# Kernel optimization log

Hardware: AMD Instinct MI355X
Metric: run time of the kernel (lower is better)

Reference implementation:

```python
import jax, jax.numpy as jnp
import numpy as np

N = 50000        # nodes
E = 800000       # edges (before self-loops)
F_IN = 128       # num_features
HID = 32         # hidden_size per head
HEADS = 4
CLS = 40         # num_classes
NEG_SLOPE = 0.2  # PyG GATConv default leaky_relu slope


def setup_inputs() -> dict:
    key = jax.random.key(0)
    ks = jax.random.split(key, 10)
    s = lambda k, sh: (jax.random.normal(k, sh, jnp.float32) * 0.05)
    x = jax.random.normal(ks[0], (N, F_IN), jnp.float32)
    edge_index = jax.random.randint(ks[1], (2, E), 0, N, dtype=jnp.int64)
    W1 = s(ks[2], (F_IN, HEADS * HID))
    att_src1 = s(ks[3], (HEADS, HID))
    att_dst1 = s(ks[4], (HEADS, HID))
    b1 = jnp.zeros((HEADS * HID,), jnp.float32)
    W2 = s(ks[5], (HEADS * HID, CLS))
    att_src2 = s(ks[6], (1, CLS))
    att_dst2 = s(ks[7], (1, CLS))
    b2 = jnp.zeros((CLS,), jnp.float32)
    return {"x": x, "edge_index": edge_index, "W1": W1, "att_src1": att_src1,
            "att_dst1": att_dst1, "b1": b1, "W2": W2, "att_src2": att_src2,
            "att_dst2": att_dst2, "b2": b2}


def _add_self_loops(edge_index, num_nodes):
    ar = jnp.arange(num_nodes, dtype=edge_index.dtype)
    loops = jnp.stack([ar, ar])
    return jnp.concatenate([edge_index, loops], axis=1)


def _gat_conv(x, edge_index, W, a_src, a_dst, bias, heads, concat):
    """PyG GATConv (eval mode, additive attention, self-loops already added)."""
    n = x.shape[0]
    src, dst = edge_index[0], edge_index[1]
    h = (x @ W).reshape(n, heads, -1)                 # [N, H, C]
    a_s = jnp.einsum('nhc,hc->nh', h, a_src)          # [N, H]
    a_d = jnp.einsum('nhc,hc->nh', h, a_dst)          # [N, H]
    e = jax.nn.leaky_relu(a_s[src] + a_d[dst], NEG_SLOPE)   # [E', H]
    m = jax.ops.segment_max(e, dst, num_segments=n)   # segment softmax over dst
    ex = jnp.exp(e - m[dst])
    den = jax.ops.segment_sum(ex, dst, num_segments=n)
    alpha = ex / den[dst]                             # [E', H]
    out = jax.ops.segment_sum(h[src] * alpha[:, :, None], dst, num_segments=n)
    out = out.reshape(n, -1) if concat else out.mean(axis=1)
    return out + bias


def reference(x, edge_index, W1, att_src1, att_dst1, b1, W2, att_src2, att_dst2, b2):
    ei = _add_self_loops(edge_index, x.shape[0])
    # dropout p=0 in eval -> identity
    h = jax.nn.relu(_gat_conv(x, ei, W1, att_src1, att_dst1, b1, HEADS, True))
    out = _gat_conv(h, ei, W2, att_src2, att_dst2, b2, 1, True)  # heads=1
    return out
```

## Files before the change

kernel.cpp:

```cpp
#include <hip/hip_runtime.h>
#include <cstdint>

#define NODES 50000
#define FIN   128
#define C1    128
#define HEADS 4
#define HID   32
#define CLS   40
#define SLOPE 0.2f

#define NBUCK ((NODES + 255) >> 8)
#define EPB 2048
#define BCAP 8192

__device__ __forceinline__ float lrelu(float v) { return v > 0.f ? v : SLOPE * v; }

__device__ __forceinline__ unsigned short f2bf(float f) {
    union { float f; unsigned u; } v; v.f = f;
    unsigned u = v.u;
    return (unsigned short)((u + 0x7FFFu + ((u >> 16) & 1u)) >> 16);
}
__device__ __forceinline__ float bf2f(unsigned short b) {
    union { unsigned u; float f; } v; v.u = ((unsigned)b) << 16;
    return v.f;
}
__device__ __forceinline__ float bflo(unsigned u) {
    union { unsigned x; float f; } v; v.x = u << 16; return v.f;
}
__device__ __forceinline__ float bfhi(unsigned u) {
    union { unsigned x; float f; } v; v.x = u & 0xffff0000u; return v.f;
}
__device__ __forceinline__ unsigned cvtpk(float a, float b) {
    unsigned r;
    asm("v_cvt_pk_bf16_f32 %0, %1, %2" : "=v"(r) : "v"(a), "v"(b));
    return r;
}

typedef __attribute__((ext_vector_type(8))) short bf16x8;
typedef __attribute__((ext_vector_type(4))) float f32x4;
typedef __attribute__((ext_vector_type(4), aligned(4))) int int4a;
typedef __attribute__((ext_vector_type(2), aligned(4))) int int2a;

__device__ __forceinline__ void acc8(float w, uint4 p, float* ac) {
    ac[0] = fmaf(w, bflo(p.x), ac[0]); ac[1] = fmaf(w, bfhi(p.x), ac[1]);
    ac[2] = fmaf(w, bflo(p.y), ac[2]); ac[3] = fmaf(w, bfhi(p.y), ac[3]);
    ac[4] = fmaf(w, bflo(p.z), ac[4]); ac[5] = fmaf(w, bfhi(p.z), ac[5]);
    ac[6] = fmaf(w, bflo(p.w), ac[6]); ac[7] = fmaf(w, bfhi(p.w), ac[7]);
}

__global__ __launch_bounds__(256) void k_prep(const float* __restrict__ W1,
                                              const float* __restrict__ W2,
                                              unsigned short* __restrict__ w1t,
                                              unsigned short* __restrict__ w2t,
                                              int* __restrict__ bwp) {
    const int b = blockIdx.x, t = threadIdx.x;
    if (b < 8) {
        __shared__ unsigned short Tb[16][136];
        const int n0 = b * 16;
        const int k = t & 127, g = t >> 7;
#pragma unroll
        for (int i = 0; i < 8; i++)
            Tb[g * 8 + i][k] = f2bf(W1[(size_t)k * C1 + n0 + g * 8 + i]);
        __syncthreads();
        {
            int nl = t >> 4, k8 = (t & 15) * 8;
            *(uint4*)(w1t + (n0 + nl) * 128 + k8) = *(uint4*)(&Tb[nl][k8]);
        }
    } else {
        for (int p = t; p < CLS * 128; p += 256) {
            int n = p >> 7, k = p & 127;
            w2t[n * 128 + k] = f2bf(W2[(size_t)k * CLS + n]);
        }
        if (t < NBUCK) bwp[t] = t * BCAP;
    }
}

__global__ __launch_bounds__(256) void k_front(const float* __restrict__ X,
                                               const unsigned short* __restrict__ w1t,
                                               const float* __restrict__ AS,
                                               const float* __restrict__ AD,
                                               unsigned short* __restrict__ h1b,
                                               float* __restrict__ as1,
                                               float* __restrict__ ad1,
                                               const int* __restrict__ src,
                                               const int* __restrict__ dst, int E,
                                               int* __restrict__ bwp,
                                               int* __restrict__ tmp, int GB1) {
    __shared__ unsigned short Asm[64][136];
    __shared__ unsigned short Wt[128][136];
    __shared__ int cnt[NBUCK];
    __shared__ int bbs[NBUCK];
    const int t = threadIdx.x;

    if (blockIdx.x >= GB1) {
        for (int i = t; i < NBUCK; i += 256) cnt[i] = 0;
        __syncthreads();
        const int e0 = (blockIdx.x - GB1) * EPB;
        int v[8], rb[8];
#pragma unroll
        for (int k = 0; k < 8; k++) {
            int e = e0 + k * 256 + t;
            rb[k] = -1;
            if (e < E) {
                int d = dst[e], s = src[e];
                int b = d >> 8;
                int r = atomicAdd(&cnt[b], 1);
                v[k] = (s << 8) | (d & 255);
                rb[k] = (r << 8) | b;
            }
        }
        __syncthreads();
        for (int i = t; i < NBUCK; i += 256) {
            int c = cnt[i];
            bbs[i] = c ? atomicAdd(&bwp[i], c) : 0;
        }
        __syncthreads();
#pragma unroll
        for (int k = 0; k < 8; k++) {
            if (rb[k] >= 0) {
                int b = rb[k] & 255;
                int r = rb[k] >> 8;
                tmp[bbs[b] + r] = v[k];
            }
        }
        return;
    }

    const int row0 = blockIdx.x * 64;
#pragma unroll
    for (int i = 0; i < 8; i++) {
        int p = i * 256 + t;
        int n = p >> 4, k8 = (p & 15) * 8;
        *(uint4*)(&Wt[n][k8]) = *(const uint4*)(w1t + n * 128 + k8);
    }
    {
        int r = t >> 2, c0 = (t & 3) * 32;
        int gr = row0 + r;
        if (gr < NODES) {
#pragma unroll
            for (int i = 0; i < 4; i++) {
                float4 va = *(const float4*)(X + (size_t)gr * FIN + c0 + i * 8);
                float4 vb = *(const float4*)(X + (size_t)gr * FIN + c0 + i * 8 + 4);
                uint4 pk;
                pk.x = cvtpk(va.x, va.y);
                pk.y = cvtpk(va.z, va.w);
                pk.z = cvtpk(vb.x, vb.y);
                pk.w = cvtpk(vb.z, vb.w);
                *(uint4*)(&Asm[r][c0 + i * 8]) = pk;
            }
        } else {
            uint4 z = make_uint4(0, 0, 0, 0);
#pragma unroll
            for (int i = 0; i < 4; i++) *(uint4*)(&Asm[r][c0 + i * 8]) = z;
        }
    }
    __syncthreads();

    const int w = t >> 6, l = t & 63;
    const int lm = l & 15, quad = l >> 4;
    f32x4 acc[8];
#pragma unroll
    for (int ct = 0; ct < 8; ct++) acc[ct] = (f32x4){0.f, 0.f, 0.f, 0.f};
#pragma unroll
    for (int kt = 0; kt < 4; kt++) {
        bf16x8 a = *(const bf16x8*)(&Asm[w * 16 + lm][kt * 32 + quad * 8]);
#pragma unroll
        for (int ct = 0; ct < 8; ct++) {
            bf16x8 b = *(const bf16x8*)(&Wt[ct * 16 + lm][kt * 32 + quad * 8]);
            acc[ct] = __builtin_amdgcn_mfma_f32_16x16x32_bf16(a, b, acc[ct], 0, 0, 0);
        }
    }
    __syncthreads();
#pragma unroll
    for (int ct = 0; ct < 8; ct++)
#pragma unroll
        for (int r = 0; r < 4; r++)
            Asm[w * 16 + quad * 4 + r][ct * 16 + lm] = f2bf(acc[ct][r]);
    __syncthreads();
    {
        int r = t >> 2, c0 = (t & 3) * 32;
        int gr = row0 + r;
        if (gr < NODES) {
#pragma unroll
            for (int i = 0; i < 4; i++)
                *(uint4*)(h1b + (size_t)gr * C1 + c0 + i * 8) =
                    *(uint4*)(&Asm[r][c0 + i * 8]);
        }
    }
    {
        int r = t >> 2, h = t & 3;
        int gr = row0 + r;
        if (gr < NODES) {
            float s = 0.f, d = 0.f;
#pragma unroll
            for (int j = 0; j < 32; j++) {
                float v = bf2f(Asm[r][h * 32 + j]);
                s = fmaf(v, AS[h * HID + j], s);
                d = fmaf(v, AD[h * HID + j], d);
            }
            as1[gr * HEADS + h] = s;
            ad1[gr * HEADS + h] = d;
        }
    }
}

__global__ __launch_bounds__(256) void k_bucketB(const int* __restrict__ bwp,
                                                 const int* __restrict__ tmp,
                                                 int* __restrict__ col,
                                                 int* __restrict__ rowptr,
                                                 int* __restrict__ degarr) {
    __shared__ int degs[256];
    __shared__ int wp[256];
    __shared__ int wsum[4];
    const int b = blockIdx.x, t = threadIdx.x;
    const int n0 = b << 8;
    const int beg = b * BCAP;
    const int end = bwp[b];
    degs[t] = 0;
    __syncthreads();
    for (int e = beg + t; e < end; e += 256)
        atomicAdd(&degs[tmp[e] & 255], 1);
    __syncthreads();
    const int d = degs[t];
    int incl = d;
    const int lane = t & 63, w = t >> 6;
#pragma unroll
    for (int s = 1; s < 64; s <<= 1) {
        int u = __shfl_up(incl, s);
        if (lane >= s) incl += u;
    }
    if (lane == 63) wsum[w] = incl;
    __syncthreads();
    if (t == 0) {
        int r = 0;
#pragma unroll
        for (int i = 0; i < 4; i++) { int x = wsum[i]; wsum[i] = r; r += x; }
    }
    __syncthreads();
    const int excl = incl - d + wsum[w] + beg;
    const int nidx = n0 + t;
    if (nidx < NODES) { rowptr[nidx] = excl; degarr[nidx] = d; }
    wp[t] = excl;
    __syncthreads();
    for (int e = beg + t; e < end; e += 256) {
        int v = tmp[e];
        int p = atomicAdd(&wp[v & 255], 1);
        col[p] = v >> 8;
    }
}

__global__ __launch_bounds__(256) void k_agg1(const unsigned short* __restrict__ h1b,
                                              const float* __restrict__ as1,
                                              const float* __restrict__ ad1,
                                              const int* __restrict__ rowptr,
                                              const int* __restrict__ degarr,
                                              const int* __restrict__ col,
                                              const float* __restrict__ b1,
                                              unsigned short* __restrict__ out1) {
    int wid = (blockIdx.x * 256 + threadIdx.x) >> 6;
    if (wid >= NODES) return;
    const int lane = threadIdx.x & 63;
    const int q  = lane >> 4;
    const int ll = lane & 15;
    const int fh = ll >> 2;
    const int n = wid;
    const float adn = ad1[n * HEADS + fh];
    const int rs = rowptr[n];
    const int re = rs + degarr[n];
    const unsigned lo = (unsigned)(ll << 4);

    float den = 0.f;
    float ac[8];
#pragma unroll
    for (int k = 0; k < 8; k++) ac[k] = 0.f;

    int base = rs;
    for (; re - base > 16; base += 32) {
        int4a ca = *(const int4a*)(col + base + q * 4);
        int4a cb = *(const int4a*)(col + base + 16 + q * 4);
        const int ia = base + q * 4;
        const int ib = base + 16 + q * 4;
        int c0 = (ia + 0 < re) ? ca.x : n;
        int c1 = (ia + 1 < re) ? ca.y : n;
        int c2 = (ia + 2 < re) ? ca.z : n;
        int c3 = (ia + 3 < re) ? ca.w : n;
        int c4 = (ib + 0 < re) ? cb.x : n;
        int c5 = (ib + 1 < re) ? cb.y : n;
        int c6 = (ib + 2 < re) ? cb.z : n;
        int c7 = (ib + 3 < re) ? cb.w : n;
        float w0 = __expf(lrelu(as1[c0 * HEADS + fh] + adn)); if (ia + 0 >= re) w0 = 0.f;
        float w1 = __expf(lrelu(as1[c1 * HEADS + fh] + adn)); if (ia + 1 >= re) w1 = 0.f;
        float w2 = __expf(lrelu(as1[c2 * HEADS + fh] + adn)); if (ia + 2 >= re) w2 = 0.f;
        float w3 = __expf(lrelu(as1[c3 * HEADS + fh] + adn)); if (ia + 3 >= re) w3 = 0.f;
        float w4 = __expf(lrelu(as1[c4 * HEADS + fh] + adn)); if (ib + 0 >= re) w4 = 0.f;
        float w5 = __expf(lrelu(as1[c5 * HEADS + fh] + adn)); if (ib + 1 >= re) w5 = 0.f;
        float w6 = __expf(lrelu(as1[c6 * HEADS + fh] + adn)); if (ib + 2 >= re) w6 = 0.f;
        float w7 = __expf(lrelu(as1[c7 * HEADS + fh] + adn)); if (ib + 3 >= re) w7 = 0.f;
        den += ((w0 + w1) + (w2 + w3)) + ((w4 + w5) + (w6 + w7));
        uint4 p0 = *(const uint4*)((const char*)h1b + (((unsigned)c0 << 8) + lo));
        uint4 p1 = *(const uint4*)((const char*)h1b + (((unsigned)c1 << 8) + lo));
        uint4 p2 = *(const uint4*)((const char*)h1b + (((unsigned)c2 << 8) + lo));
        uint4 p3 = *(const uint4*)((const char*)h1b + (((unsigned)c3 << 8) + lo));
        uint4 p4 = *(const uint4*)((const char*)h1b + (((unsigned)c4 << 8) + lo));
        uint4 p5 = *(const uint4*)((const char*)h1b + (((unsigned)c5 << 8) + lo));
        uint4 p6 = *(const uint4*)((const char*)h1b + (((unsigned)c6 << 8) + lo));
        uint4 p7 = *(const uint4*)((const char*)h1b + (((unsigned)c7 << 8) + lo));
        acc8(w0, p0, ac); acc8(w1, p1, ac); acc8(w2, p2, ac); acc8(w3, p3, ac);
        acc8(w4, p4, ac); acc8(w5, p5, ac); acc8(w6, p6, ac); acc8(w7, p7, ac);
    }
    if (base < re) {
        int4a ca = *(const int4a*)(col + base + q * 4);
        const int ia = base + q * 4;
        int c0 = (ia + 0 < re) ? ca.x : n;
        int c1 = (ia + 1 < re) ? ca.y : n;
        int c2 = (ia + 2 < re) ? ca.z : n;
        int c3 = (ia + 3 < re) ? ca.w : n;
        float w0 = __expf(lrelu(as1[c0 * HEADS + fh] + adn)); if (ia + 0 >= re) w0 = 0.f;
        float w1 = __expf(lrelu(as1[c1 * HEADS + fh] + adn)); if (ia + 1 >= re) w1 = 0.f;
        float w2 = __expf(lrelu(as1[c2 * HEADS + fh] + adn)); if (ia + 2 >= re) w2 = 0.f;
        float w3 = __expf(lrelu(as1[c3 * HEADS + fh] + adn)); if (ia + 3 >= re) w3 = 0.f;
        den += (w0 + w1) + (w2 + w3);
        uint4 p0 = *(const uint4*)((const char*)h1b + (((unsigned)c0 << 8) + lo));
        uint4 p1 = *(const uint4*)((const char*)h1b + (((unsigned)c1 << 8) + lo));
        uint4 p2 = *(const uint4*)((const char*)h1b + (((unsigned)c2 << 8) + lo));
        uint4 p3 = *(const uint4*)((const char*)h1b + (((unsigned)c3 << 8) + lo));
        acc8(w0, p0, ac); acc8(w1, p1, ac); acc8(w2, p2, ac); acc8(w3, p3, ac);
    }
    den += __shfl_xor(den, 16);
    den += __shfl_xor(den, 32);
#pragma unroll
    for (int k = 0; k < 8; k++) {
        ac[k] += __shfl_xor(ac[k], 16);
        ac[k] += __shfl_xor(ac[k], 32);
    }
    const float wself = __expf(lrelu(as1[n * HEADS + fh] + adn));
    den += wself;
    if (q == 0) {
        unsigned offs = ((unsigned)n << 8) + lo;
        uint4 sp = *(const uint4*)((const char*)h1b + offs);
        float sv[8] = {bflo(sp.x), bfhi(sp.x), bflo(sp.y), bfhi(sp.y),
                       bflo(sp.z), bfhi(sp.z), bflo(sp.w), bfhi(sp.w)};
        float4 bv0 = *(const float4*)(b1 + ll * 8);
        float4 bv1 = *(const float4*)(b1 + ll * 8 + 4);
        float bb[8] = {bv0.x, bv0.y, bv0.z, bv0.w, bv1.x, bv1.y, bv1.z, bv1.w};
        const float inv = 1.f / den;
        float o[8];
#pragma unroll
        for (int k = 0; k < 8; k++)
            o[k] = fmaxf(fmaf(wself, sv[k], ac[k]) * inv + bb[k], 0.f);
        uint4 pk;
        pk.x = cvtpk(o[0], o[1]);
        pk.y = cvtpk(o[2], o[3]);
        pk.z = cvtpk(o[4], o[5]);
        pk.w = cvtpk(o[6], o[7]);
        *(uint4*)(out1 + (size_t)n * C1 + ll * 8) = pk;
    }
}

__global__ __launch_bounds__(256) void k_gemm2(const unsigned short* __restrict__ out1b,
                                               const unsigned short* __restrict__ w2t,
                                               const float* __restrict__ AS,
                                               const float* __restrict__ AD,
                                               unsigned short* __restrict__ h2b,
                                               float* __restrict__ as2,
                                               float* __restrict__ ad2) {
    __shared__ unsigned short Asm[64][136];
    __shared__ unsigned short Wt2[48][136];
    __shared__ float Cc[64][52];
    const int t = threadIdx.x;
    const int row0 = blockIdx.x * 64;

    for (int p = t; p < 8 * 136; p += 256) Wt2[40 + p / 136][p % 136] = 0;
    for (int p = t; p < 640; p += 256) {
        int n = p >> 4, k8 = (p & 15) * 8;
        *(uint4*)(&Wt2[n][k8]) = *(const uint4*)(w2t + n * 128 + k8);
    }
    {
        int r = t >> 2, c0 = (t & 3) * 32;
        int gr = row0 + r;
        if (gr < NODES) {
#pragma unroll
            for (int i = 0; i < 4; i++)
                *(uint4*)(&Asm[r][c0 + i * 8]) =
                    *(const uint4*)(out1b + (size_t)gr * C1 + c0 + i * 8);
        } else {
            uint4 z = make_uint4(0, 0, 0, 0);
#pragma unroll
            for (int i = 0; i < 4; i++) *(uint4*)(&Asm[r][c0 + i * 8]) = z;
        }
    }
    __syncthreads();

    const int w = t >> 6, l = t & 63;
    const int lm = l & 15, quad = l >> 4;
    f32x4 acc[3];
#pragma unroll
    for (int ct = 0; ct < 3; ct++) acc[ct] = (f32x4){0.f, 0.f, 0.f, 0.f};
#pragma unroll
    for (int kt = 0; kt < 4; kt++) {
        bf16x8 a = *(const bf16x8*)(&Asm[w * 16 + lm][kt * 32 + quad * 8]);
#pragma unroll
        for (int ct = 0; ct < 3; ct++) {
            bf16x8 b = *(const bf16x8*)(&Wt2[ct * 16 + lm][kt * 32 + quad * 8]);
            acc[ct] = __builtin_amdgcn_mfma_f32_16x16x32_bf16(a, b, acc[ct], 0, 0, 0);
        }
    }
    __syncthreads();
#pragma unroll
    for (int ct = 0; ct < 3; ct++)
#pragma unroll
        for (int r = 0; r < 4; r++)
            Cc[w * 16 + quad * 4 + r][ct * 16 + lm] = acc[ct][r];
    __syncthreads();
    {
        int r = t >> 2, c0 = (t & 3) * 10;
        int gr = row0 + r;
        if (gr < NODES) {
#pragma unroll
            for (int i = 0; i < 5; i++) {
                int c = c0 + i * 2;
                unsigned pk = cvtpk(Cc[r][c], Cc[r][c + 1]);
                *(unsigned*)(h2b + (size_t)gr * 64 + c) = pk;
            }
            float s = 0.f, d = 0.f;
#pragma unroll
            for (int j = 0; j < 10; j++) {
                float v = Cc[r][c0 + j];
                s = fmaf(v, AS[c0 + j], s);
                d = fmaf(v, AD[c0 + j], d);
            }
            s += __shfl_xor(s, 1); s += __shfl_xor(s, 2);
            d += __shfl_xor(d, 1); d += __shfl_xor(d, 2);
            if ((t & 3) == 0) { as2[gr] = s; ad2[gr] = d; }
        }
    }
}

__global__ __launch_bounds__(256) void k_agg2(const unsigned short* __restrict__ h2b,
                                              const float* __restrict__ as2,
                                              const float* __restrict__ ad2,
                                              const int* __restrict__ rowptr,
                                              const int* __restrict__ degarr,
                                              const int* __restrict__ col,
                                              const float* __restrict__ b2,
                                              float* __restrict__ out) {
    int wid = (blockIdx.x * 256 + threadIdx.x) >> 6;
    if (wid >= NODES) return;
    const int lane = threadIdx.x & 63;
    const int q8 = lane >> 3, l8 = lane & 7;
    const int n = wid;
    const float adn = ad2[n];
    const int rs = rowptr[n];
    const int re = rs + degarr[n];
    const unsigned lo = (unsigned)(l8 << 4);

    float den = 0.f;
    float ac[8];
#pragma unroll
    for (int k = 0; k < 8; k++) ac[k] = 0.f;

    int base = rs;
    for (; re - base > 16; base += 32) {
        int4a cc = *(const int4a*)(col + base + q8 * 4);
        const int i0 = base + q8 * 4;
        int c0 = (i0 + 0 < re) ? cc.x : n;
        int c1 = (i0 + 1 < re) ? cc.y : n;
        int c2 = (i0 + 2 < re) ? cc.z : n;
        int c3 = (i0 + 3 < re) ? cc.w : n;
        float w0 = __expf(lrelu(as2[c0] + adn)); if (i0 + 0 >= re) w0 = 0.f;
        float w1 = __expf(lrelu(as2[c1] + adn)); if (i0 + 1 >= re) w1 = 0.f;
        float w2 = __expf(lrelu(as2[c2] + adn)); if (i0 + 2 >= re) w2 = 0.f;
        float w3 = __expf(lrelu(as2[c3] + adn)); if (i0 + 3 >= re) w3 = 0.f;
        den += (w0 + w1) + (w2 + w3);
        if (l8 < 5) {
            uint4 p0 = *(const uint4*)((const char*)h2b + (((unsigned)c0 << 7) + lo));
            uint4 p1 = *(const uint4*)((const char*)h2b + (((unsigned)c1 << 7) + lo));
            uint4 p2 = *(const uint4*)((const char*)h2b + (((unsigned)c2 << 7) + lo));
            uint4 p3 = *(const uint4*)((const char*)h2b + (((unsigned)c3 << 7) + lo));
            acc8(w0, p0, ac); acc8(w1, p1, ac);
            acc8(w2, p2, ac); acc8(w3, p3, ac);
        }
    }
    if (base < re) {
        int2a cc = *(const int2a*)(col + base + q8 * 2);
        const int i0 = base + q8 * 2;
        int c0 = (i0 + 0 < re) ? cc.x : n;
        int c1 = (i0 + 1 < re) ? cc.y : n;
        float w0 = __expf(lrelu(as2[c0] + adn)); if (i0 + 0 >= re) w0 = 0.f;
        float w1 = __expf(lrelu(as2[c1] + adn)); if (i0 + 1 >= re) w1 = 0.f;
        den += w0 + w1;
        if (l8 < 5) {
            uint4 p0 = *(const uint4*)((const char*)h2b + (((unsigned)c0 << 7) + lo));
            uint4 p1 = *(const uint4*)((const char*)h2b + (((unsigned)c1 << 7) + lo));
            acc8(w0, p0, ac); acc8(w1, p1, ac);
        }
    }
    den += __shfl_xor(den, 8);
    den += __shfl_xor(den, 16);
    den += __shfl_xor(den, 32);
#pragma unroll
    for (int k = 0; k < 8; k++) {
        ac[k] += __shfl_xor(ac[k], 8);
        ac[k] += __shfl_xor(ac[k], 16);
        ac[k] += __shfl_xor(ac[k], 32);
    }
    const float wself = __expf(lrelu(as2[n] + adn));
    den += wself;
    if (q8 == 0 && l8 < 5) {
        unsigned offs = ((unsigned)n << 7) + lo;
        uint4 sp = *(const uint4*)((const char*)h2b + offs);
        float sv[8] = {bflo(sp.x), bfhi(sp.x), bflo(sp.y), bfhi(sp.y),
                       bflo(sp.z), bfhi(sp.z), bflo(sp.w), bfhi(sp.w)};
        float4 bv0 = *(const float4*)(b2 + l8 * 8);
        float4 bv1 = *(const float4*)(b2 + l8 * 8 + 4);
        float bb[8] = {bv0.x, bv0.y, bv0.z, bv0.w, bv1.x, bv1.y, bv1.z, bv1.w};
        float o[8];
#pragma unroll
        for (int k = 0; k < 8; k++)
            o[k] = (ac[k] + wself * sv[k]) / den + bb[k];
        *(float4*)(out + (size_t)n * CLS + l8 * 8) =
            make_float4(o[0], o[1], o[2], o[3]);
        *(float4*)(out + (size_t)n * CLS + l8 * 8 + 4) =
            make_float4(o[4], o[5], o[6], o[7]);
    }
}

extern "C" void kernel_launch(void* const* d_in, const int* in_sizes, int n_in,
                              void* d_out, int out_size, void* d_ws, size_t ws_size,
                              hipStream_t stream) {
    const float* x     = (const float*)d_in[0];
    const int*   ei    = (const int*)d_in[1];
    const float* W1    = (const float*)d_in[2];
    const float* aS1   = (const float*)d_in[3];
    const float* aD1   = (const float*)d_in[4];
    const float* b1    = (const float*)d_in[5];
    const float* W2    = (const float*)d_in[6];
    const float* aS2   = (const float*)d_in[7];
    const float* aD2   = (const float*)d_in[8];
    const float* b2    = (const float*)d_in[9];
    float* out = (float*)d_out;
    const int E = in_sizes[1] / 2;
    const int* src = ei;
    const int* dst = ei + E;

    char* ws = (char*)d_ws;
    size_t off = 0;
    auto alloc = [&](size_t bytes) -> char* {
        char* p = ws + off;
        off += (bytes + 255) & ~(size_t)255;
        return p;
    };
    unsigned short* h1b  = (unsigned short*)alloc((size_t)NODES * C1 * 2);
    unsigned short* out1 = (unsigned short*)alloc((size_t)NODES * C1 * 2);
    unsigned short* h2b  = (unsigned short*)alloc((size_t)NODES * 64 * 2);
    float* as1    = (float*)alloc((size_t)NODES * HEADS * 4);
    float* ad1    = (float*)alloc((size_t)NODES * HEADS * 4);
    float* as2    = (float*)alloc((size_t)NODES * 4);
    float* ad2    = (float*)alloc((size_t)NODES * 4);
    int* rowptr   = (int*)alloc((size_t)NODES * 4);
    int* degarr   = (int*)alloc((size_t)NODES * 4);
    int* col      = (int*)alloc((size_t)NBUCK * BCAP * 4 + 256);
    int* tmp      = (int*)alloc((size_t)NBUCK * BCAP * 4 + 256);
    unsigned short* w1t = (unsigned short*)alloc((size_t)FIN * C1 * 2);
    unsigned short* w2t = (unsigned short*)alloc((size_t)CLS * 128 * 2);
    int* bwp      = (int*)alloc((size_t)NBUCK * 4);

    const int GB1 = (NODES + 63) / 64;
    const int GBA = (E + EPB - 1) / EPB;

    k_prep<<<9, 256, 0, stream>>>(W1, W2, w1t, w2t, bwp);
    k_front<<<GB1 + GBA, 256, 0, stream>>>(x, w1t, aS1, aD1, h1b, as1, ad1,
                                           src, dst, E, bwp, tmp, GB1);
    k_bucketB<<<NBUCK, 256, 0, stream>>>(bwp, tmp, col, rowptr, degarr);
    k_agg1<<<(NODES * 64) / 256, 256, 0, stream>>>(h1b, as1, ad1, rowptr, degarr,
                                                   col, b1, out1);
    k_gemm2<<<(NODES + 63) / 64, 256, 0, stream>>>(out1, w2t, aS2, aD2, h2b, as2, ad2);
    k_agg2<<<(NODES * 64) / 256, 256, 0, stream>>>(h2b, as2, ad2, rowptr, degarr,
                                                   col, b2, out);
}
```

Baseline: 193.7 us.

## Compact h2 row stride, widen bucket kernel, vectorize attention dot products

Result: faster. 189.7 us, median of 2 (-2.0%).

```diff
diff --git a/kernel.cpp b/kernel.cpp
--- a/kernel.cpp
+++ b/kernel.cpp
@@ -193,10 +193,22 @@
         if (gr < NODES) {
             float s = 0.f, d = 0.f;
 #pragma unroll
-            for (int j = 0; j < 32; j++) {
-                float v = bf2f(Asm[r][h * 32 + j]);
-                s = fmaf(v, AS[h * HID + j], s);
-                d = fmaf(v, AD[h * HID + j], d);
+            for (int i = 0; i < 4; i++) {
+                uint4 hv = *(const uint4*)(&Asm[r][h * 32 + i * 8]);
+                float4 a0 = *(const float4*)(AS + h * HID + i * 8);
+                float4 a1 = *(const float4*)(AS + h * HID + i * 8 + 4);
+                float4 d0 = *(const float4*)(AD + h * HID + i * 8);
+                float4 d1 = *(const float4*)(AD + h * HID + i * 8 + 4);
+                float v0 = bflo(hv.x), v1 = bfhi(hv.x), v2 = bflo(hv.y), v3 = bfhi(hv.y);
+                float v4 = bflo(hv.z), v5 = bfhi(hv.z), v6 = bflo(hv.w), v7 = bfhi(hv.w);
+                s = fmaf(v0, a0.x, s); s = fmaf(v1, a0.y, s);
+                s = fmaf(v2, a0.z, s); s = fmaf(v3, a0.w, s);
+                s = fmaf(v4, a1.x, s); s = fmaf(v5, a1.y, s);
+                s = fmaf(v6, a1.z, s); s = fmaf(v7, a1.w, s);
+                d = fmaf(v0, d0.x, d); d = fmaf(v1, d0.y, d);
+                d = fmaf(v2, d0.z, d); d = fmaf(v3, d0.w, d);
+                d = fmaf(v4, d1.x, d); d = fmaf(v5, d1.y, d);
+                d = fmaf(v6, d1.z, d); d = fmaf(v7, d1.w, d);
             }
             as1[gr * HEADS + h] = s;
             ad1[gr * HEADS + h] = d;
@@ -204,7 +216,7 @@
     }
 }
 
-__global__ __launch_bounds__(256) void k_bucketB(const int* __restrict__ bwp,
+__global__ __launch_bounds__(512) void k_bucketB(const int* __restrict__ bwp,
                                                  const int* __restrict__ tmp,
                                                  int* __restrict__ col,
                                                  int* __restrict__ rowptr,
@@ -216,20 +228,23 @@
     const int n0 = b << 8;
     const int beg = b * BCAP;
     const int end = bwp[b];
-    degs[t] = 0;
-    __syncthreads();
-    for (int e = beg + t; e < end; e += 256)
+    if (t < 256) degs[t] = 0;
+    __syncthreads();
+    for (int e = beg + t; e < end; e += 512)
         atomicAdd(&degs[tmp[e] & 255], 1);
     __syncthreads();
-    const int d = degs[t];
-    int incl = d;
+    int d = 0, incl = 0;
     const int lane = t & 63, w = t >> 6;
-#pragma unroll
-    for (int s = 1; s < 64; s <<= 1) {
-        int u = __shfl_up(incl, s);
-        if (lane >= s) incl += u;
-    }
-    if (lane == 63) wsum[w] = incl;
+    if (t < 256) {
+        d = degs[t];
+        incl = d;
+#pragma unroll
+        for (int s = 1; s < 64; s <<= 1) {
+            int u = __shfl_up(incl, s);
+            if (lane >= s) incl += u;
+        }
+        if (lane == 63) wsum[w] = incl;
+    }
     __syncthreads();
     if (t == 0) {
         int r = 0;
@@ -237,12 +252,14 @@
         for (int i = 0; i < 4; i++) { int x = wsum[i]; wsum[i] = r; r += x; }
     }
     __syncthreads();
-    const int excl = incl - d + wsum[w] + beg;
-    const int nidx = n0 + t;
-    if (nidx < NODES) { rowptr[nidx] = excl; degarr[nidx] = d; }
-    wp[t] = excl;
-    __syncthreads();
-    for (int e = beg + t; e < end; e += 256) {
+    if (t < 256) {
+        const int excl = incl - d + wsum[w] + beg;
+        const int nidx = n0 + t;
+        if (nidx < NODES) { rowptr[nidx] = excl; degarr[nidx] = d; }
+        wp[t] = excl;
+    }
+    __syncthreads();
+    for (int e = beg + t; e < end; e += 512) {
         int v = tmp[e];
         int p = atomicAdd(&wp[v & 255], 1);
         col[p] = v >> 8;
@@ -420,7 +437,7 @@
             for (int i = 0; i < 5; i++) {
                 int c = c0 + i * 2;
                 unsigned pk = cvtpk(Cc[r][c], Cc[r][c + 1]);
-                *(unsigned*)(h2b + (size_t)gr * 64 + c) = pk;
+                *(unsigned*)(h2b + (size_t)gr * 40 + c) = pk;
             }
             float s = 0.f, d = 0.f;
 #pragma unroll
@@ -473,10 +490,10 @@
         float w3 = __expf(lrelu(as2[c3] + adn)); if (i0 + 3 >= re) w3 = 0.f;
         den += (w0 + w1) + (w2 + w3);
         if (l8 < 5) {
-            uint4 p0 = *(const uint4*)((const char*)h2b + (((unsigned)c0 << 7) + lo));
-            uint4 p1 = *(const uint4*)((const char*)h2b + (((unsigned)c1 << 7) + lo));
-            uint4 p2 = *(const uint4*)((const char*)h2b + (((unsigned)c2 << 7) + lo));
-            uint4 p3 = *(const uint4*)((const char*)h2b + (((unsigned)c3 << 7) + lo));
+            uint4 p0 = *(const uint4*)((const char*)h2b + ((unsigned)c0 * 80u + lo));
+            uint4 p1 = *(const uint4*)((const char*)h2b + ((unsigned)c1 * 80u + lo));
+            uint4 p2 = *(const uint4*)((const char*)h2b + ((unsigned)c2 * 80u + lo));
+            uint4 p3 = *(const uint4*)((const char*)h2b + ((unsigned)c3 * 80u + lo));
             acc8(w0, p0, ac); acc8(w1, p1, ac);
             acc8(w2, p2, ac); acc8(w3, p3, ac);
         }
@@ -490,8 +507,8 @@
         float w1 = __expf(lrelu(as2[c1] + adn)); if (i0 + 1 >= re) w1 = 0.f;
         den += w0 + w1;
         if (l8 < 5) {
-            uint4 p0 = *(const uint4*)((const char*)h2b + (((unsigned)c0 << 7) + lo));
-            uint4 p1 = *(const uint4*)((const char*)h2b + (((unsigned)c1 << 7) + lo));
+            uint4 p0 = *(const uint4*)((const char*)h2b + ((unsigned)c0 * 80u + lo));
+            uint4 p1 = *(const uint4*)((const char*)h2b + ((unsigned)c1 * 80u + lo));
             acc8(w0, p0, ac); acc8(w1, p1, ac);
         }
     }
@@ -507,7 +524,7 @@
     const float wself = __expf(lrelu(as2[n] + adn));
     den += wself;
     if (q8 == 0 && l8 < 5) {
-        unsigned offs = ((unsigned)n << 7) + lo;
+        unsigned offs = (unsigned)n * 80u + lo;
         uint4 sp = *(const uint4*)((const char*)h2b + offs);
         float sv[8] = {bflo(sp.x), bfhi(sp.x), bflo(sp.y), bfhi(sp.y),
                        bflo(sp.z), bfhi(sp.z), bflo(sp.w), bfhi(sp.w)};
@@ -552,15 +569,15 @@
     };
     unsigned short* h1b  = (unsigned short*)alloc((size_t)NODES * C1 * 2);
     unsigned short* out1 = (unsigned short*)alloc((size_t)NODES * C1 * 2);
-    unsigned short* h2b  = (unsigned short*)alloc((size_t)NODES * 64 * 2);
+    unsigned short* h2b  = (unsigned short*)alloc((size_t)NODES * 40 * 2);
     float* as1    = (float*)alloc((size_t)NODES * HEADS * 4);
     float* ad1    = (float*)alloc((size_t)NODES * HEADS * 4);
     float* as2    = (float*)alloc((size_t)NODES * 4);
     float* ad2    = (float*)alloc((size_t)NODES * 4);
     int* rowptr   = (int*)alloc((size_t)NODES * 4);
     int* degarr   = (int*)alloc((size_t)NODES * 4);
-    int* col      = (int*)alloc((size_t)NBUCK * BCAP * 4 + 256);
-    int* tmp      = (int*)alloc((size_t)NBUCK * BCAP * 4 + 256);
+    int* col      = (int*)alloc((size_t)NBUCK * BCAP * 4 + 1024);
+    int* tmp      = (int*)alloc((size_t)NBUCK * BCAP * 4 + 1024);
     unsigned short* w1t = (unsigned short*)alloc((size_t)FIN * C1 * 2);
     unsigned short* w2t = (unsigned short*)alloc((size_t)CLS * 128 * 2);
     int* bwp      = (int*)alloc((size_t)NBUCK * 4);
@@ -571,7 +588,7 @@
     k_prep<<<9, 256, 0, stream>>>(W1, W2, w1t, w2t, bwp);
     k_front<<<GB1 + GBA, 256, 0, stream>>>(x, w1t, aS1, aD1, h1b, as1, ad1,
                                            src, dst, E, bwp, tmp, GB1);
-    k_bucketB<<<NBUCK, 256, 0, stream>>>(bwp, tmp, col, rowptr, degarr);
+    k_bucketB<<<NBUCK, 512, 0, stream>>>(bwp, tmp, col, rowptr, degarr);
     k_agg1<<<(NODES * 64) / 256, 256, 0, stream>>>(h1b, as1, ad1, rowptr, degarr,
                                                    col, b1, out1);
     k_gemm2<<<(NODES + 63) / 64, 256, 0, stream>>>(out1, w2t, aS2, aD2, h2b, as2, ad2);
```
